# Optimization experiments

Hardware: AMD Instinct MI355X
Metric: run time of the kernel (lower is better)

The kernel has to match this reference:

```python
import jax, jax.numpy as jnp
import numpy as np

SIZE = 256  # matrix dimension n; input vector length = n*(n-1)/2
BATCH = 512

# strictly-lower indices in the same row-major (i, j<i) order as the module's l_indices
_ROWS, _COLS = np.tril_indices(SIZE, k=-1)


def setup_inputs() -> dict:
    key = jax.random.key(0)
    m = SIZE * (SIZE - 1) // 2
    # z entries are partial-correlation-like values, must lie in (-1, 1)
    vec = jax.random.uniform(key, (BATCH, m), dtype=jnp.float32, minval=-0.99, maxval=0.99)
    return {"vec": vec}


def reference(vec):
    B = vec.shape[0]
    n = SIZE
    # scatter vector into strictly-lower triangle: (B, n, n)
    z = jnp.zeros((B, n, n), dtype=vec.dtype).at[:, _ROWS, _COLS].set(vec)
    signs = jnp.sign(z)
    signs = jnp.where(signs == 0, jnp.asarray(1.0, vec.dtype), signs)
    z2 = z * z

    row_idx = jnp.arange(n)  # (n,)

    def step(rowsum, inp):
        # rowsum: (B, n) running sum of x_squared over already-built columns, per row
        j, z2_col = inp  # z2_col: (B, n) = z^2[:, :, j]
        base = z2_col * (1.0 - rowsum)           # lower entries (rows > j)
        col = jnp.where(row_idx[None, :] == j, jnp.asarray(1.0, vec.dtype),
                        jnp.where(row_idx[None, :] < j, jnp.asarray(0.0, vec.dtype), base))
        return rowsum + col, col

    z2_cols = jnp.moveaxis(z2, -1, 0)  # (n_col, B, n_row)
    _, x2_cols = jax.lax.scan(step, jnp.zeros((B, n), dtype=vec.dtype),
                              (jnp.arange(n), z2_cols))
    # x2_cols: (n_col, B, n_row) -> (B, n_row, n_col)
    x2 = jnp.moveaxis(x2_cols, 0, -1)
    return jnp.sqrt(x2) * signs
```

## Files before the change

kernel.cpp:

```cpp
#include <hip/hip_runtime.h>


#define SIZE 256
#define BATCH 512
#define M (SIZE * (SIZE - 1) / 2)
#define TOTAL (BATCH * M)

typedef float f4u __attribute__((ext_vector_type(4), aligned(4)));

template <int CTRL, int ROW_MASK>
__device__ __forceinline__ float scan_mul(float p) {
    int sh = __builtin_amdgcn_update_dpp(
        __builtin_bit_cast(int, 1.0f),
        __builtin_bit_cast(int, p),
        CTRL, ROW_MASK, 0xF, false);
    return p * __builtin_bit_cast(float, sh);
}

__device__ __forceinline__ float excl_shift_one(float p) {
    int r = __builtin_amdgcn_update_dpp(
        __builtin_bit_cast(int, 1.0f),
        __builtin_bit_cast(int, p),
        0x138 , 0xF, 0xF, false);
    return __builtin_bit_cast(float, r);
}

__global__ __launch_bounds__(256) void chol_from_z_kernel(
    const float* __restrict__ vec, float* __restrict__ out) {
    const int lane = threadIdx.x & 63;
    const int wib = __builtin_amdgcn_readfirstlane((int)threadIdx.x >> 6);
    const int wave = (int)blockIdx.x * 4 + wib;
    const int b = wave >> 8;
    const int i = wave & 255;
    const int row_off = b * M + ((i * (i - 1)) >> 1);
    const float* __restrict__ s = vec + row_off;
    float* __restrict__ dst = out + ((size_t)wave << 8);
    const int j0 = lane << 2;

    const int maxidx = (TOTAL - 1) - row_off;
    f4u zv;
    if (j0 + 3 <= maxidx) {
        zv = *(const f4u*)(s + j0);
    } else {
        zv.x = s[j0]; zv.y = s[j0 + 1]; zv.z = s[j0 + 2]; zv.w = 0.f;
    }

    const float z0 = (j0     < i) ? zv.x : 0.f;
    const float z1 = (j0 + 1 < i) ? zv.y : 0.f;
    const float z2 = (j0 + 2 < i) ? zv.z : 0.f;
    const float z3 = (j0 + 3 < i) ? zv.w : 0.f;

    const float t0 = 1.f - z0 * z0;
    const float t1 = 1.f - z1 * z1;
    const float t2 = 1.f - z2 * z2;
    const float t3 = 1.f - z3 * z3;

    float p = (t0 * t1) * (t2 * t3);

    p = scan_mul<0x111, 0xF>(p);
    p = scan_mul<0x112, 0xF>(p);
    p = scan_mul<0x114, 0xF>(p);
    p = scan_mul<0x118, 0xF>(p);
    if (i >= 64)  p = scan_mul<0x142, 0xA>(p);
    if (i >= 128) p = scan_mul<0x143, 0xC>(p);

    float run = excl_shift_one(p);

    f4u o;
    o.x = (j0     == i) ? 1.f : z0 * __builtin_amdgcn_sqrtf(run); run *= t0;
    o.y = (j0 + 1 == i) ? 1.f : z1 * __builtin_amdgcn_sqrtf(run); run *= t1;
    o.z = (j0 + 2 == i) ? 1.f : z2 * __builtin_amdgcn_sqrtf(run); run *= t2;
    o.w = (j0 + 3 == i) ? 1.f : z3 * __builtin_amdgcn_sqrtf(run);

    *(f4u*)(dst + j0) = o;
}

extern "C" void kernel_launch(void* const* d_in, const int* in_sizes, int n_in,
                              void* d_out, int out_size, void* d_ws, size_t ws_size,
                              hipStream_t stream) {
    const float* vec = (const float*)d_in[0];
    float* out = (float*)d_out;
    const int n_waves = BATCH * SIZE;
    const int blocks = n_waves / 4;
    chol_from_z_kernel<<<blocks, 256, 0, stream>>>(vec, out);
}
```

Before: 174.8 us.

## Process sixteen batch rows per wave with software-prefetched next chunk

Each wave now handles the same matrix row i for 16 batch entries, strided by 32, instead of a single row. The load for the next batch entry is issued before the current one is computed, so memory latency can overlap with compute. The grid shrinks to 8192 waves and the launch bounds gain an occupancy hint. Fewer waves means less parallelism to hide latency; the wrapped prefetch on the last iteration also issues one redundant load per wave.

```diff
diff --git a/kernel.cpp b/kernel.cpp
--- a/kernel.cpp
+++ b/kernel.cpp
@@ -5,6 +5,8 @@
 #define BATCH 512
 #define M (SIZE * (SIZE - 1) / 2)
 #define TOTAL (BATCH * M)
+#define NWAVES 8192
+#define ROWS_PER_WAVE 16
 
 typedef float f4u __attribute__((ext_vector_type(4), aligned(4)));
 
@@ -25,54 +27,70 @@
     return __builtin_bit_cast(float, r);
 }
 
-__global__ __launch_bounds__(256) void chol_from_z_kernel(
+__device__ __forceinline__ f4u load_chunk(const float* __restrict__ vec,
+                                          int row_off, int j0) {
+    const float* __restrict__ s = vec + row_off;
+    f4u zv;
+    if (row_off <= TOTAL - 256) {
+        zv = *(const f4u*)(s + j0);
+    } else {
+        const int mi = TOTAL - 1 - row_off;
+        zv.x = s[j0     < mi ? j0     : mi];
+        zv.y = s[j0 + 1 < mi ? j0 + 1 : mi];
+        zv.z = s[j0 + 2 < mi ? j0 + 2 : mi];
+        zv.w = s[j0 + 3 < mi ? j0 + 3 : mi];
+    }
+    return zv;
+}
+
+__global__ __launch_bounds__(256, 8) void chol_from_z_kernel(
     const float* __restrict__ vec, float* __restrict__ out) {
     const int lane = threadIdx.x & 63;
     const int wib = __builtin_amdgcn_readfirstlane((int)threadIdx.x >> 6);
-    const int wave = (int)blockIdx.x * 4 + wib;
-    const int b = wave >> 8;
-    const int i = wave & 255;
-    const int row_off = b * M + ((i * (i - 1)) >> 1);
-    const float* __restrict__ s = vec + row_off;
-    float* __restrict__ dst = out + ((size_t)wave << 8);
+    const int wave_id = (int)blockIdx.x * 4 + wib;
+    const int i  = wave_id & 255;
+    const int b0 = wave_id >> 8;
+    const int tri = (i * (i - 1)) >> 1;
     const int j0 = lane << 2;
 
-    const int maxidx = (TOTAL - 1) - row_off;
-    f4u zv;
-    if (j0 + 3 <= maxidx) {
-        zv = *(const f4u*)(s + j0);
-    } else {
-        zv.x = s[j0]; zv.y = s[j0 + 1]; zv.z = s[j0 + 2]; zv.w = 0.f;
+    f4u zv = load_chunk(vec, b0 * M + tri, j0);
+
+    for (int k = 0; k < ROWS_PER_WAVE; ++k) {
+        const int b = b0 + (k << 5);
+        const int bn = (k == ROWS_PER_WAVE - 1) ? b0 : b + 32;
+        f4u znext = load_chunk(vec, bn * M + tri, j0);
+
+        const float z0 = (j0     < i) ? zv.x : 0.f;
+        const float z1 = (j0 + 1 < i) ? zv.y : 0.f;
+        const float z2 = (j0 + 2 < i) ? zv.z : 0.f;
+        const float z3 = (j0 + 3 < i) ? zv.w : 0.f;
+
+        const float t0 = 1.f - z0 * z0;
+        const float t1 = 1.f - z1 * z1;
+        const float t2 = 1.f - z2 * z2;
+        const float t3 = 1.f - z3 * z3;
+
+        float p = (t0 * t1) * (t2 * t3);
+        p = scan_mul<0x111, 0xF>(p);
+        p = scan_mul<0x112, 0xF>(p);
+        p = scan_mul<0x114, 0xF>(p);
+        p = scan_mul<0x118, 0xF>(p);
+        if (i >= 64)  p = scan_mul<0x142, 0xA>(p);
+        if (i >= 128) p = scan_mul<0x143, 0xC>(p);
+
+        float run = excl_shift_one(p);
+
+        f4u o;
+        o.x = (j0     == i) ? 1.f : z0 * __builtin_amdgcn_sqrtf(run); run *= t0;
+        o.y = (j0 + 1 == i) ? 1.f : z1 * __builtin_amdgcn_sqrtf(run); run *= t1;
+        o.z = (j0 + 2 == i) ? 1.f : z2 * __builtin_amdgcn_sqrtf(run); run *= t2;
+        o.w = (j0 + 3 == i) ? 1.f : z3 * __builtin_amdgcn_sqrtf(run);
+
+        float* __restrict__ dst = out + (((size_t)b << 8) + (size_t)i) * SIZE + j0;
+        *(f4u*)dst = o;
+
+        zv = znext;
     }
-
-    const float z0 = (j0     < i) ? zv.x : 0.f;
-    const float z1 = (j0 + 1 < i) ? zv.y : 0.f;
-    const float z2 = (j0 + 2 < i) ? zv.z : 0.f;
-    const float z3 = (j0 + 3 < i) ? zv.w : 0.f;
-
-    const float t0 = 1.f - z0 * z0;
-    const float t1 = 1.f - z1 * z1;
-    const float t2 = 1.f - z2 * z2;
-    const float t3 = 1.f - z3 * z3;
-
-    float p = (t0 * t1) * (t2 * t3);
-
-    p = scan_mul<0x111, 0xF>(p);
-    p = scan_mul<0x112, 0xF>(p);
-    p = scan_mul<0x114, 0xF>(p);
-    p = scan_mul<0x118, 0xF>(p);
-    if (i >= 64)  p = scan_mul<0x142, 0xA>(p);
-    if (i >= 128) p = scan_mul<0x143, 0xC>(p);
-
-    float run = excl_shift_one(p);
-
-    f4u o;
-    o.x = (j0     == i) ? 1.f : z0 * __builtin_amdgcn_sqrtf(run); run *= t0;
-    o.y = (j0 + 1 == i) ? 1.f : z1 * __builtin_amdgcn_sqrtf(run); run *= t1;
-    o.z = (j0 + 2 == i) ? 1.f : z2 * __builtin_amdgcn_sqrtf(run); run *= t2;
-    o.w = (j0 + 3 == i) ? 1.f : z3 * __builtin_amdgcn_sqrtf(run);
-
-    *(f4u*)(dst + j0) = o;
 }
 
 extern "C" void kernel_launch(void* const* d_in, const int* in_sizes, int n_in,
@@ -80,7 +98,5 @@
                               hipStream_t stream) {
     const float* vec = (const float*)d_in[0];
     float* out = (float*)d_out;
-    const int n_waves = BATCH * SIZE;
-    const int blocks = n_waves / 4;
-    chol_from_z_kernel<<<blocks, 256, 0, stream>>>(vec, out);
+    chol_from_z_kernel<<<NWAVES / 4, 256, 0, stream>>>(vec, out);
 }
```

After: 184.0 us. 5.3% more time.
